# Kernel optimization log

Measured on AMD Instinct MI355X. Metric: run time of the kernel, lower is better.

The kernel has to match this reference:

```python
import jax, jax.numpy as jnp
import numpy as np

INPUT_DIM = 256
OUTPUT_DIM = 512
NUM_KNOTS = 64
RANGE_KNOTS = (-1.0, 1.0)
DEGREE = 3
BATCH = 4096


def bspline_basis(x, knots, degree):
    """Cox-de Boor recursion. x: [B, I], knots: [K] (uniform, ascending).
    Returns basis values [B, I, K - degree - 1]."""
    xe = x[..., None]  # [B, I, 1]
    # degree-0: indicator of knot interval k, k = 0..K-2
    basis = ((xe >= knots[:-1]) & (xe < knots[1:])).astype(x.dtype)  # [B, I, K-1]
    for d in range(1, degree + 1):
        k = np.arange(knots.shape[0] - d - 1)
        left = (xe - knots[k]) / (knots[k + d] - knots[k]) * basis[..., :-1]
        right = (knots[k + d + 1] - xe) / (knots[k + d + 1] - knots[k + 1]) * basis[..., 1:]
        basis = left + right  # [B, I, K-d-1]
    return basis


def setup_inputs() -> dict:
    key = jax.random.key(0)
    kx, kb, ks = jax.random.split(key, 3)
    x = jax.random.uniform(kx, (BATCH, INPUT_DIM), dtype=jnp.float32)
    wb = jax.random.uniform(kb, (INPUT_DIM, OUTPUT_DIM), dtype=jnp.float32)
    ws = jax.random.uniform(ks, (INPUT_DIM, OUTPUT_DIM), dtype=jnp.float32)
    cps = jnp.ones((INPUT_DIM, NUM_KNOTS), dtype=jnp.float32)
    knots = jnp.asarray(np.linspace(RANGE_KNOTS[0], RANGE_KNOTS[1], NUM_KNOTS), dtype=jnp.float32)
    return {"x": x, "wb": wb, "ws": ws, "cps": cps, "knots": knots}


def reference(x, wb, ws, cps, knots):
    num_basis = NUM_KNOTS - DEGREE - 1
    basis = bspline_basis(x, knots, DEGREE)            # [B, I, num_basis]
    # per-input-dim spline value: sum_k cps[i, k] * B_k(x[b, i])
    spline = jnp.einsum('bik,ik->bi', basis, cps[:, :num_basis])  # [B, I]
    base = jax.nn.silu(x)                               # [B, I]
    # out[b, o] = sum_i wb[i, o] * silu(x[b, i]) + ws[i, o] * spline[b, i]
    out = base @ wb + spline @ ws                       # [B, O]
    return out
```

## Files before the change

kernel.cpp:

```cpp
#include <hip/hip_runtime.h>
#include <hip/hip_bf16.h>

#define BATCH    4096
#define IN_DIM   256
#define OUT_DIM  512
#define KDIM     512
#define NKNOTS   64
#define NBASIS   60

typedef __attribute__((ext_vector_type(8))) short bf16x8;
typedef __attribute__((ext_vector_type(4))) float f32x4;

__device__ __forceinline__ short f2bf(float f) {
    __hip_bfloat16 h = __float2bfloat16(f);
    return *reinterpret_cast<short*>(&h);
}

__global__ __launch_bounds__(256) void prep_a_kernel(
        const float* __restrict__ x, const float* __restrict__ cps,
        const float* __restrict__ knots, short* __restrict__ A) {
    int idx = blockIdx.x * 256 + threadIdx.x;
    int b = idx >> 8;
    int i = idx & (IN_DIM - 1);

    float xv = x[idx];
    float base = xv / (1.0f + __expf(-xv));

    float u = (xv + 1.0f) * 31.5f;
    int   j = (int)floorf(u);
    float spline = 0.0f;
    if (j >= 0 && j <= 62) {
        float t  = (xv - knots[j]) * 31.5f;
        float t2 = t * t, t3 = t2 * t;
        float omt = 1.0f - t;
        const float c6 = 1.0f / 6.0f;
        float w0 = omt * omt * omt * c6;
        float w1 = (3.0f*t3 - 6.0f*t2 + 4.0f) * c6;
        float w2 = (-3.0f*t3 + 3.0f*t2 + 3.0f*t + 1.0f) * c6;
        float w3 = t3 * c6;
        const float* cp = cps + i * NKNOTS;
        int k0 = j - 3;
        if (k0     >= 0 && k0     < NBASIS) spline += w0 * cp[k0];
        if (k0 + 1 >= 0 && k0 + 1 < NBASIS) spline += w1 * cp[k0 + 1];
        if (k0 + 2 >= 0 && k0 + 2 < NBASIS) spline += w2 * cp[k0 + 2];
        if (k0 + 3 >= 0 && k0 + 3 < NBASIS) spline += w3 * cp[k0 + 3];
    }

    A[b * KDIM + i]          = f2bf(base);
    A[b * KDIM + IN_DIM + i] = f2bf(spline);
}

__global__ __launch_bounds__(256) void prep_b_kernel(
        const float* __restrict__ wb, const float* __restrict__ ws,
        short* __restrict__ Bt) {
    int idx = blockIdx.x * 256 + threadIdx.x;
    int n = idx >> 9;
    int k = idx & (KDIM - 1);
    float v = (k < IN_DIM) ? wb[k * OUT_DIM + n] : ws[(k - IN_DIM) * OUT_DIM + n];
    Bt[idx] = f2bf(v);
}

#define BM 64
#define BN 64
#define BK 64
#define LDSS 72

__global__ __launch_bounds__(256) void gemm_kernel(
        const short* __restrict__ A, const short* __restrict__ Bt,
        float* __restrict__ C) {
    __shared__ __align__(16) short As[BM * LDSS];
    __shared__ __align__(16) short Bs[BN * LDSS];

    const int m0 = blockIdx.y * BM;
    const int n0 = blockIdx.x * BN;
    const int tid  = threadIdx.x;
    const int lane = tid & 63;
    const int wave = tid >> 6;
    const int wm = (wave & 1) * 32;
    const int wn = (wave >> 1) * 32;
    const int fr   = lane & 15;
    const int koff = (lane >> 4) * 8;

    f32x4 acc[2][2] = {};

    const int c1 = tid, c2 = tid + 256;
    const int r1 = c1 >> 3, o1 = (c1 & 7) * 8;
    const int r2 = c2 >> 3, o2 = (c2 & 7) * 8;

    for (int k0 = 0; k0 < KDIM; k0 += BK) {
        *(uint4*)&As[r1 * LDSS + o1] = *(const uint4*)&A[(m0 + r1) * KDIM + k0 + o1];
        *(uint4*)&As[r2 * LDSS + o2] = *(const uint4*)&A[(m0 + r2) * KDIM + k0 + o2];
        *(uint4*)&Bs[r1 * LDSS + o1] = *(const uint4*)&Bt[(n0 + r1) * KDIM + k0 + o1];
        *(uint4*)&Bs[r2 * LDSS + o2] = *(const uint4*)&Bt[(n0 + r2) * KDIM + k0 + o2];
        __syncthreads();

        #pragma unroll
        for (int kk = 0; kk < BK; kk += 32) {
            bf16x8 a0 = *(const bf16x8*)&As[(wm + fr)      * LDSS + kk + koff];
            bf16x8 a1 = *(const bf16x8*)&As[(wm + 16 + fr) * LDSS + kk + koff];
            bf16x8 b0 = *(const bf16x8*)&Bs[(wn + fr)      * LDSS + kk + koff];
            bf16x8 b1 = *(const bf16x8*)&Bs[(wn + 16 + fr) * LDSS + kk + koff];
            acc[0][0] = __builtin_amdgcn_mfma_f32_16x16x32_bf16(a0, b0, acc[0][0], 0, 0, 0);
            acc[0][1] = __builtin_amdgcn_mfma_f32_16x16x32_bf16(a0, b1, acc[0][1], 0, 0, 0);
            acc[1][0] = __builtin_amdgcn_mfma_f32_16x16x32_bf16(a1, b0, acc[1][0], 0, 0, 0);
            acc[1][1] = __builtin_amdgcn_mfma_f32_16x16x32_bf16(a1, b1, acc[1][1], 0, 0, 0);
        }
        __syncthreads();
    }

    const int rbase = (lane >> 4) * 4;
    #pragma unroll
    for (int mt = 0; mt < 2; ++mt) {
        #pragma unroll
        for (int nt = 0; nt < 2; ++nt) {
            #pragma unroll
            for (int r = 0; r < 4; ++r) {
                int row = m0 + wm + mt * 16 + rbase + r;
                int col = n0 + wn + nt * 16 + fr;
                C[row * OUT_DIM + col] = acc[mt][nt][r];
            }
        }
    }
}

extern "C" void kernel_launch(void* const* d_in, const int* in_sizes, int n_in,
                              void* d_out, int out_size, void* d_ws, size_t ws_size,
                              hipStream_t stream) {
    const float* x     = (const float*)d_in[0];
    const float* wb    = (const float*)d_in[1];
    const float* ws    = (const float*)d_in[2];
    const float* cps   = (const float*)d_in[3];
    const float* knots = (const float*)d_in[4];
    float* out = (float*)d_out;

    short* Abf = (short*)d_ws;
    short* Btb = (short*)((char*)d_ws + (size_t)BATCH * KDIM * 2);

    prep_a_kernel<<<BATCH * IN_DIM / 256, 256, 0, stream>>>(x, cps, knots, Abf);
    prep_b_kernel<<<OUT_DIM * KDIM / 256, 256, 0, stream>>>(wb, ws, Btb);

    dim3 grid(OUT_DIM / BN, BATCH / BM);
    gemm_kernel<<<grid, 256, 0, stream>>>(Abf, Btb, out);
}
```

Before: 85.41 us.

## Fuse prep and GEMM into one cooperative kernel with grid syncs

Replaces the three kernel launches (A prep, B transpose, GEMM) with a single cooperative kernel of 512 blocks. The kernel stages bf16 operands inside the output buffer, synchronises the whole grid, runs an LDS-free MFMA GEMM that reads operands directly from global memory, synchronises again, then overwrites the output. It also vectorises the A prep to 8 elements per thread and computes the spline fraction from u instead of loading knots. The aim is to remove launch overhead and LDS staging, at the cost of two grid-wide barriers, uncoalesced global operand loads and an occupancy limit of 512 co-resident blocks.

```diff
diff --git a/kernel.cpp b/kernel.cpp
--- a/kernel.cpp
+++ b/kernel.cpp
@@ -1,5 +1,6 @@
 #include <hip/hip_runtime.h>
 #include <hip/hip_bf16.h>
+#include <hip/hip_cooperative_groups.h>
 
 #define BATCH    4096
 #define IN_DIM   256
@@ -16,97 +17,95 @@
     return *reinterpret_cast<short*>(&h);
 }
 
-__global__ __launch_bounds__(256) void prep_a_kernel(
-        const float* __restrict__ x, const float* __restrict__ cps,
-        const float* __restrict__ knots, short* __restrict__ A) {
-    int idx = blockIdx.x * 256 + threadIdx.x;
-    int b = idx >> 8;
-    int i = idx & (IN_DIM - 1);
+__global__ __launch_bounds__(256) void fused_kan(
+        const float* __restrict__ x, const float* __restrict__ wb,
+        const float* __restrict__ ws, const float* __restrict__ cps,
+        const float* __restrict__ knots, float* out) {
+    (void)knots;
 
-    float xv = x[idx];
-    float base = xv / (1.0f + __expf(-xv));
+    short* Abf = (short*)out;
+    short* Btb = Abf + (size_t)BATCH * KDIM;
 
-    float u = (xv + 1.0f) * 31.5f;
-    int   j = (int)floorf(u);
-    float spline = 0.0f;
-    if (j >= 0 && j <= 62) {
-        float t  = (xv - knots[j]) * 31.5f;
-        float t2 = t * t, t3 = t2 * t;
-        float omt = 1.0f - t;
-        const float c6 = 1.0f / 6.0f;
-        float w0 = omt * omt * omt * c6;
-        float w1 = (3.0f*t3 - 6.0f*t2 + 4.0f) * c6;
-        float w2 = (-3.0f*t3 + 3.0f*t2 + 3.0f*t + 1.0f) * c6;
-        float w3 = t3 * c6;
-        const float* cp = cps + i * NKNOTS;
-        int k0 = j - 3;
-        if (k0     >= 0 && k0     < NBASIS) spline += w0 * cp[k0];
-        if (k0 + 1 >= 0 && k0 + 1 < NBASIS) spline += w1 * cp[k0 + 1];
-        if (k0 + 2 >= 0 && k0 + 2 < NBASIS) spline += w2 * cp[k0 + 2];
-        if (k0 + 3 >= 0 && k0 + 3 < NBASIS) spline += w3 * cp[k0 + 3];
+    const int tid = threadIdx.x;
+    const int g   = blockIdx.x * 256 + tid;
+
+    {
+        const int b  = g >> 5;
+        const int i0 = (g & 31) << 3;
+        float xv[8];
+        *(f32x4*)&xv[0] = *(const f32x4*)&x[b * IN_DIM + i0];
+        *(f32x4*)&xv[4] = *(const f32x4*)&x[b * IN_DIM + i0 + 4];
+        bf16x8 sil, spl;
+        #pragma unroll
+        for (int e = 0; e < 8; ++e) {
+            float v = xv[e];
+            float s = v / (1.0f + __expf(-v));
+            float u  = (v + 1.0f) * 31.5f;
+            float fj = floorf(u);
+            int   j  = (int)fj;
+            float sp = 0.0f;
+            if (j >= 0 && j <= 62) {
+                float t  = u - fj;
+                float t2 = t * t, t3 = t2 * t;
+                float omt = 1.0f - t;
+                const float c6 = 1.0f / 6.0f;
+                float w0 = omt * omt * omt * c6;
+                float w1 = (3.0f*t3 - 6.0f*t2 + 4.0f) * c6;
+                float w2 = (-3.0f*t3 + 3.0f*t2 + 3.0f*t + 1.0f) * c6;
+                float w3 = t3 * c6;
+                const float* cp = cps + (i0 + e) * NKNOTS;
+                int k0 = j - 3;
+                if (k0     >= 0 && k0     < NBASIS) sp += w0 * cp[k0];
+                if (k0 + 1 >= 0 && k0 + 1 < NBASIS) sp += w1 * cp[k0 + 1];
+                if (k0 + 2 >= 0 && k0 + 2 < NBASIS) sp += w2 * cp[k0 + 2];
+                if (               k0 + 3 < NBASIS) sp += w3 * cp[k0 + 3];
+            }
+            sil[e] = f2bf(s);
+            spl[e] = f2bf(sp);
+        }
+        *(bf16x8*)&Abf[b * KDIM + i0]          = sil;
+        *(bf16x8*)&Abf[b * KDIM + IN_DIM + i0] = spl;
     }
 
-    A[b * KDIM + i]          = f2bf(base);
-    A[b * KDIM + IN_DIM + i] = f2bf(spline);
-}
+    {
+        const int n  = g & 511;
+        const int kq = g >> 9;
+        Btb[n * KDIM + kq]          = f2bf(wb[kq * OUT_DIM + n]);
+        Btb[n * KDIM + IN_DIM + kq] = f2bf(ws[kq * OUT_DIM + n]);
+    }
 
-__global__ __launch_bounds__(256) void prep_b_kernel(
-        const float* __restrict__ wb, const float* __restrict__ ws,
-        short* __restrict__ Bt) {
-    int idx = blockIdx.x * 256 + threadIdx.x;
-    int n = idx >> 9;
-    int k = idx & (KDIM - 1);
-    float v = (k < IN_DIM) ? wb[k * OUT_DIM + n] : ws[(k - IN_DIM) * OUT_DIM + n];
-    Bt[idx] = f2bf(v);
-}
+    cooperative_groups::this_grid().sync();
 
-#define BM 64
-#define BN 64
-#define BK 64
-#define LDSS 72
-
-__global__ __launch_bounds__(256) void gemm_kernel(
-        const short* __restrict__ A, const short* __restrict__ Bt,
-        float* __restrict__ C) {
-    __shared__ __align__(16) short As[BM * LDSS];
-    __shared__ __align__(16) short Bs[BN * LDSS];
-
-    const int m0 = blockIdx.y * BM;
-    const int n0 = blockIdx.x * BN;
-    const int tid  = threadIdx.x;
+    const int bid  = blockIdx.x;
+    const int sbid = (bid & 7) * 64 + (bid >> 3);
+    const int n0   = (sbid & 7) * 64;
+    const int m0   = (sbid >> 3) * 64;
     const int lane = tid & 63;
     const int wave = tid >> 6;
-    const int wm = (wave & 1) * 32;
-    const int wn = (wave >> 1) * 32;
+    const int wm   = (wave & 1) * 32;
+    const int wn   = (wave >> 1) * 32;
     const int fr   = lane & 15;
     const int koff = (lane >> 4) * 8;
 
+    const short* A0 = Abf + (size_t)(m0 + wm + fr) * KDIM + koff;
+    const short* A1 = A0 + 16 * KDIM;
+    const short* B0 = Btb + (size_t)(n0 + wn + fr) * KDIM + koff;
+    const short* B1 = B0 + 16 * KDIM;
+
     f32x4 acc[2][2] = {};
+    #pragma unroll 4
+    for (int k = 0; k < KDIM; k += 32) {
+        bf16x8 a0 = *(const bf16x8*)(A0 + k);
+        bf16x8 a1 = *(const bf16x8*)(A1 + k);
+        bf16x8 b0 = *(const bf16x8*)(B0 + k);
+        bf16x8 b1 = *(const bf16x8*)(B1 + k);
+        acc[0][0] = __builtin_amdgcn_mfma_f32_16x16x32_bf16(a0, b0, acc[0][0], 0, 0, 0);
+        acc[0][1] = __builtin_amdgcn_mfma_f32_16x16x32_bf16(a0, b1, acc[0][1], 0, 0, 0);
+        acc[1][0] = __builtin_amdgcn_mfma_f32_16x16x32_bf16(a1, b0, acc[1][0], 0, 0, 0);
+        acc[1][1] = __builtin_amdgcn_mfma_f32_16x16x32_bf16(a1, b1, acc[1][1], 0, 0, 0);
+    }
 
-    const int c1 = tid, c2 = tid + 256;
-    const int r1 = c1 >> 3, o1 = (c1 & 7) * 8;
-    const int r2 = c2 >> 3, o2 = (c2 & 7) * 8;
-
-    for (int k0 = 0; k0 < KDIM; k0 += BK) {
-        *(uint4*)&As[r1 * LDSS + o1] = *(const uint4*)&A[(m0 + r1) * KDIM + k0 + o1];
-        *(uint4*)&As[r2 * LDSS + o2] = *(const uint4*)&A[(m0 + r2) * KDIM + k0 + o2];
-        *(uint4*)&Bs[r1 * LDSS + o1] = *(const uint4*)&Bt[(n0 + r1) * KDIM + k0 + o1];
-        *(uint4*)&Bs[r2 * LDSS + o2] = *(const uint4*)&Bt[(n0 + r2) * KDIM + k0 + o2];
-        __syncthreads();
-
-        #pragma unroll
-        for (int kk = 0; kk < BK; kk += 32) {
-            bf16x8 a0 = *(const bf16x8*)&As[(wm + fr)      * LDSS + kk + koff];
-            bf16x8 a1 = *(const bf16x8*)&As[(wm + 16 + fr) * LDSS + kk + koff];
-            bf16x8 b0 = *(const bf16x8*)&Bs[(wn + fr)      * LDSS + kk + koff];
-            bf16x8 b1 = *(const bf16x8*)&Bs[(wn + 16 + fr) * LDSS + kk + koff];
-            acc[0][0] = __builtin_amdgcn_mfma_f32_16x16x32_bf16(a0, b0, acc[0][0], 0, 0, 0);
-            acc[0][1] = __builtin_amdgcn_mfma_f32_16x16x32_bf16(a0, b1, acc[0][1], 0, 0, 0);
-            acc[1][0] = __builtin_amdgcn_mfma_f32_16x16x32_bf16(a1, b0, acc[1][0], 0, 0, 0);
-            acc[1][1] = __builtin_amdgcn_mfma_f32_16x16x32_bf16(a1, b1, acc[1][1], 0, 0, 0);
-        }
-        __syncthreads();
-    }
+    cooperative_groups::this_grid().sync();
 
     const int rbase = (lane >> 4) * 4;
     #pragma unroll
@@ -117,7 +116,7 @@
             for (int r = 0; r < 4; ++r) {
                 int row = m0 + wm + mt * 16 + rbase + r;
                 int col = n0 + wn + nt * 16 + fr;
-                C[row * OUT_DIM + col] = acc[mt][nt][r];
+                out[row * OUT_DIM + col] = acc[mt][nt][r];
             }
         }
     }
@@ -126,19 +125,16 @@
 extern "C" void kernel_launch(void* const* d_in, const int* in_sizes, int n_in,
                               void* d_out, int out_size, void* d_ws, size_t ws_size,
                               hipStream_t stream) {
+    (void)in_sizes; (void)n_in; (void)d_ws; (void)ws_size; (void)out_size;
     const float* x     = (const float*)d_in[0];
     const float* wb    = (const float*)d_in[1];
-    const float* ws    = (const float*)d_in[2];
+    const float* wsp   = (const float*)d_in[2];
     const float* cps   = (const float*)d_in[3];
     const float* knots = (const float*)d_in[4];
     float* out = (float*)d_out;
 
-    short* Abf = (short*)d_ws;
-    short* Btb = (short*)((char*)d_ws + (size_t)BATCH * KDIM * 2);
-
-    prep_a_kernel<<<BATCH * IN_DIM / 256, 256, 0, stream>>>(x, cps, knots, Abf);
-    prep_b_kernel<<<OUT_DIM * KDIM / 256, 256, 0, stream>>>(wb, ws, Btb);
-
-    dim3 grid(OUT_DIM / BN, BATCH / BM);
-    gemm_kernel<<<grid, 256, 0, stream>>>(Abf, Btb, out);
+    void* args[] = {(void*)&x, (void*)&wb, (void*)&wsp, (void*)&cps,
+                    (void*)&knots, (void*)&out};
+    hipLaunchCooperativeKernel((const void*)fused_kan, dim3(512), dim3(256),
+                               args, 0, stream);
 }
```

Result: slower. 220.1 us (+157.7%).
